# Kernel tuning notes

Hardware: AMD Instinct MI355X
Metric: run time of the kernel (lower is better)

Reference implementation:

```python
import jax, jax.numpy as jnp
import numpy as np

N, D = 16384, 32          # nodes, max neighbors
IN_F, HID, OUT_F = 128, 128, 128
HEADS = 8
HD = HID // HEADS         # head dim
TDIM = 64                 # Time2Vec dim
NORM = float(np.sqrt(1.0 / HD))


def _lin_params(key, fan_in, fan_out):
    k1, k2 = jax.random.split(key)
    lim = 1.0 / np.sqrt(fan_in)
    W = jax.random.uniform(k1, (fan_in, fan_out), jnp.float32, -lim, lim)
    b = jax.random.uniform(k2, (fan_out,), jnp.float32, -lim, lim)
    return W, b


def setup_inputs() -> dict:
    key = jax.random.key(0)
    ks = jax.random.split(key, 16)
    x = jax.random.normal(ks[0], (N, IN_F), jnp.float32)
    neighbors = jax.random.randint(ks[1], (N, D), 0, N)
    times = jax.random.uniform(ks[2], (N, D), jnp.float32)
    t = jax.random.uniform(ks[3], (1,), jnp.float32)
    # node KQV
    Wk, bk = _lin_params(ks[4], IN_F, HID)
    Wq, bq = _lin_params(ks[5], IN_F, HID)
    Wv, bv = _lin_params(ks[6], IN_F, HID)
    # Time2Vec kernel: [w0*t+b0, sin(t*W + B)] -> TDIM feats
    w0 = jax.random.normal(ks[7], (1,), jnp.float32)
    b0 = jax.random.normal(ks[8], (1,), jnp.float32)
    Wt = jax.random.normal(ks[9], (1, TDIM - 1), jnp.float32)
    Bt = jax.random.normal(ks[10], (TDIM - 1,), jnp.float32)
    # time KQV
    Wtk, btk = _lin_params(ks[11], TDIM, HID)
    Wtq, btq = _lin_params(ks[12], TDIM, HID)
    Wtv, btv = _lin_params(ks[13], TDIM, HID)
    # output MLP
    W1, b1 = _lin_params(ks[14], HID + IN_F, HID)
    W2, b2 = _lin_params(ks[15], HID, OUT_F)
    return dict(x=x, neighbors=neighbors, times=times, t=t,
                Wk=Wk, bk=bk, Wq=Wq, bq=bq, Wv=Wv, bv=bv,
                w0=w0, b0=b0, Wt=Wt, Bt=Bt,
                Wtk=Wtk, btk=btk, Wtq=Wtq, btq=btq, Wtv=Wtv, btv=btv,
                W1=W1, b1=b1, W2=W2, b2=b2)


def _t2v(ts, w0, b0, Wt, Bt):
    # ts: [..., 1] -> [..., TDIM]
    return jnp.concatenate([ts * w0 + b0, jnp.sin(ts @ Wt + Bt)], axis=-1)


def reference(x, neighbors, times, t,
              Wk, bk, Wq, bq, Wv, bv,
              w0, b0, Wt, Bt,
              Wtk, btk, Wtq, btq, Wtv, btv,
              W1, b1, W2, b2):
    t0 = t[0]
    # node-level K/Q/V for all nodes
    k_ = x @ Wk + bk
    q_ = x @ Wq + bq
    v_ = x @ Wv + bv
    # time encodings
    enc_t = _t2v(t.reshape(1, 1), w0, b0, Wt, Bt)          # [1, TDIM]
    tq = enc_t @ Wtq + btq                                  # [1, HID] (same for every target node)
    enc_nb = _t2v(times[..., None], w0, b0, Wt, Bt)        # [N, D, TDIM]
    tk = enc_nb @ Wtk + btk                                 # [N, D, HID]
    tv = enc_nb @ Wtv + btv
    # gather neighbor K/V and add time encodings
    q = q_ + tq                                             # [N, HID]
    k = k_[neighbors] + tk                                  # [N, D, HID]
    v = v_[neighbors] + tv
    # multi-head attention over (time-masked) neighbors
    qh = q.reshape(N, HEADS, HD)
    kh = k.reshape(N, D, HEADS, HD)
    vh = v.reshape(N, D, HEADS, HD)
    scores = jnp.einsum('nhd,nmhd->nhm', qh, kh) * NORM     # [N, H, D]
    mask = times <= t0                                      # [N, D]
    scores = jnp.where(mask[:, None, :], scores, -1e9)
    attn = jax.nn.softmax(scores, axis=-1)
    h = jnp.einsum('nhm,nmhd->nhd', attn, vh).reshape(N, HID)
    # nodes with no valid (time <= t) neighbors output zeros
    h = jnp.where(mask.any(axis=-1)[:, None], h, 0.0)
    # output MLP on [x || h]
    z = jnp.concatenate([x, h], axis=1)
    return jax.nn.relu(z @ W1 + b1) @ W2 + b2
```

## Files before the change

### kernel.cpp

```cpp
#include <hip/hip_runtime.h>
#include <hip/hip_bf16.h>

#define NNODES 16384

typedef unsigned short u16;
typedef unsigned int   u32;
typedef __attribute__((ext_vector_type(8))) short bf16x8;
typedef __attribute__((ext_vector_type(4))) float f32x4;

__device__ __forceinline__ float bfl(u32 u) { return __uint_as_float(u << 16); }
__device__ __forceinline__ float bfh(u32 u) { return __uint_as_float(u & 0xffff0000u); }
__device__ __forceinline__ u16 f2b(float f) {
    u32 u = __float_as_uint(f);
    return (u16)((u + 0x7fffu + ((u >> 16) & 1u)) >> 16);
}
__device__ __forceinline__ u32 pk2(float a, float b) {
    return (u32)f2b(a) | ((u32)f2b(b) << 16);
}
__device__ __forceinline__ bf16x8 bcast8(int4 v) {
    return __builtin_bit_cast(bf16x8, v);
}

#if defined(__has_builtin)
#if __has_builtin(__builtin_amdgcn_fdot2_f32_bf16)
#define HAVE_DOT2 1
#endif
#if __has_builtin(__builtin_amdgcn_sinf) && __has_builtin(__builtin_amdgcn_fractf)
#define HAVE_HWSIN 1
#endif
#endif
#ifndef HAVE_DOT2
#define HAVE_DOT2 0
#endif
#ifndef HAVE_HWSIN
#define HAVE_HWSIN 0
#endif

#if HAVE_DOT2
typedef __attribute__((ext_vector_type(2))) __bf16 bf16x2;
__device__ __forceinline__ float dot2b(u32 a, u32 b, float c) {
    return __builtin_amdgcn_fdot2_f32_bf16(__builtin_bit_cast(bf16x2, a),
                                           __builtin_bit_cast(bf16x2, b), c, false);
}
#else
__device__ __forceinline__ float dot2b(u32 a, u32 b, float c) {
    return c + bfl(a) * bfl(b) + bfh(a) * bfh(b);
}
#endif

#if HAVE_HWSIN
__device__ __forceinline__ float hwsin(float y) {
    return __builtin_amdgcn_sinf(__builtin_amdgcn_fractf(y));
}
#else
__device__ __forceinline__ float hwsin(float y) {
    return __sinf(y * 6.28318530717958647692f);
}
#endif

__global__ __launch_bounds__(256) void setup_all(
    const float* __restrict__ Wk, const float* __restrict__ Wq,
    const float* __restrict__ Wv, const float* __restrict__ W1,
    const float* __restrict__ W2,
    const float* __restrict__ t,  const float* __restrict__ bq,
    const float* __restrict__ btq,const float* __restrict__ Wtq,
    const float* __restrict__ w0, const float* __restrict__ b0,
    const float* __restrict__ Wt, const float* __restrict__ Bt,
    const float* __restrict__ Wtk,const float* __restrict__ Wtv,
    u16* __restrict__ Wts, float* __restrict__ qbias,
    float* __restrict__ gb, u32* __restrict__ Wtvp, u16* __restrict__ WGt,
    float2* __restrict__ wb2p)
{
    __shared__ float sb[128 * 17 + 64 * 17];
    int b = blockIdx.x, tt = threadIdx.x;

    if (b < 96) {
        int mat = b >> 4, tile = b & 15;
        const float* src = (mat == 0) ? Wk : (mat == 1) ? Wq : (mat == 2) ? Wv
                         : (mat == 3) ? W1 : (mat == 4) ? (W1 + 128 * 128) : W2;
        u16* dst = Wts + (size_t)mat * 16384;
        #pragma unroll
        for (int i = 0; i < 4; i++) {
            int o = i * 256 + tt;
            int cl = o >> 7, k = o & 127;
            int c = tile * 8 + cl;
            dst[c * 128 + k] = f2b(src[k * 128 + c]);
        }
    } else if (b == 96 || b == 97) {
        float tv = t[0];
        if (tt < 64)
            sb[tt] = (tt == 0) ? (w0[0] * tv + b0[0])
                               : __sinf(tv * Wt[tt - 1] + Bt[tt - 1]);
        __syncthreads();
        if (tt < 128) {
            float s = bq[tt] + btq[tt];
            for (int k = 0; k < 64; k++)
                s += sb[k] * Wtq[k * 128 + tt];
            sb[64 + tt] = s;
            if (b == 96) qbias[tt] = s;
        }
        __syncthreads();
        if (b == 97) {
            #pragma unroll
            for (int r = 0; r < 2; r++) {
                int hj = tt + r * 256;
                int h = hj >> 6, j = hj & 63;
                float s = 0.f;
                #pragma unroll
                for (int d = 0; d < 16; d++)
                    s += sb[64 + h * 16 + d] * Wtk[(size_t)j * 128 + h * 16 + d];
                gb[hj] = s;
            }
        }
    } else if (b == 98) {
        #pragma unroll
        for (int i = 0; i < 16; i++) {
            int idx = i * 256 + tt;
            int kp = idx >> 7, c = idx & 127;
            Wtvp[idx] = pk2(Wtv[(size_t)(2 * kp) * 128 + c],
                            Wtv[(size_t)(2 * kp + 1) * 128 + c]);
        }
        const float inv2pi = 0.15915494309189533577f;
        if (tt < 63) {
            float2 v;
            v.x = Wt[tt] * inv2pi;
            v.y = Bt[tt] * inv2pi;
            wb2p[tt + 1] = v;
        } else if (tt == 63) {
            float2 v;
            v.x = w0[0];
            v.y = b0[0];
            wb2p[0] = v;
        }
    } else {
        int h = b - 99;
        float* WqL  = sb;
        float* WtkL = sb + 128 * 17;
        #pragma unroll
        for (int i = 0; i < 8; i++) {
            int o = i * 256 + tt;
            int k = o >> 4, d = o & 15;
            WqL[k * 17 + d] = Wq[(size_t)k * 128 + h * 16 + d];
        }
        #pragma unroll
        for (int i = 0; i < 4; i++) {
            int o = i * 256 + tt;
            int j = o >> 4, d = o & 15;
            WtkL[j * 17 + d] = Wtk[(size_t)j * 128 + h * 16 + d];
        }
        __syncthreads();
        int j = tt >> 2, kb = (tt & 3) * 32;
        float wk[16];
        #pragma unroll
        for (int d = 0; d < 16; d++) wk[d] = WtkL[j * 17 + d];
        u32 out[16];
        #pragma unroll
        for (int kk2 = 0; kk2 < 16; kk2++) {
            int k = kb + 2 * kk2;
            float s0 = 0.f, s1 = 0.f;
            #pragma unroll
            for (int d = 0; d < 16; d++) {
                s0 += WqL[k * 17 + d] * wk[d];
                s1 += WqL[(k + 1) * 17 + d] * wk[d];
            }
            out[kk2] = pk2(s0, s1);
        }
        int4* dst = (int4*)(WGt + (size_t)(h * 64 + j) * 128 + kb);
        const int4* srcv = (const int4*)out;
        #pragma unroll
        for (int i = 0; i < 4; i++) dst[i] = srcv[i];
    }
}

__global__ __launch_bounds__(256) void gemm8m4(
    const float* __restrict__ x, const u16* __restrict__ Wts,
    const u16* __restrict__ WGt,
    const float* __restrict__ bk, const float* __restrict__ qbias,
    const float* __restrict__ bv, const float* __restrict__ b1,
    const float* __restrict__ gb,
    u16* __restrict__ Kb, u16* __restrict__ Qb,
    u16* __restrict__ Vb, u16* __restrict__ Pb, u16* __restrict__ Gb)
{
    __shared__ u16 As[64 * 128];
    __shared__ u16 Ws[128 * 128];
    int t = threadIdx.x;
    int rb = blockIdx.x * 64;
    int grp = blockIdx.y;

    u32* As32 = (u32*)As;
    u32* Ws32 = (u32*)Ws;
    const float2* Ap = (const float2*)(x + (size_t)rb * 128);
    #pragma unroll
    for (int i = 0; i < 16; i++) {
        int idx2 = i * 256 + t;
        int r = idx2 >> 6, k2 = idx2 & 63;
        float2 v = Ap[idx2];
        As32[(r * 64 + k2) ^ ((r & 7) << 2)] = pk2(v.x, v.y);
    }

    int wid = t >> 6, lane = t & 63;
    int l15 = lane & 15, lg = lane >> 4;
    int mb = wid * 16;
    int xo = (l15 & 7) << 3;

    #pragma unroll
    for (int mi = 0; mi < 4; mi++) {
        int mat = grp * 4 + mi;
        const u16* Wt = (mat < 4) ? (Wts + (size_t)mat * 16384)
                                  : (WGt + (size_t)(mat - 4) * 16384);
        const float* bias = (mat == 0) ? bk : (mat == 1) ? qbias
                          : (mat == 2) ? bv : (mat == 3) ? b1
                          : (gb + (mat - 4) * 128);
        const u32* Wp = (const u32*)Wt;
        __syncthreads();
        #pragma unroll
        for (int i = 0; i < 32; i++) {
            int idx2 = i * 256 + t;
            int c = idx2 >> 6, k2 = idx2 & 63;
            Ws32[(c * 64 + k2) ^ ((c & 7) << 2)] = Wp[idx2];
        }
        __syncthreads();

        f32x4 acc[8];
        #pragma unroll
        for (int nt = 0; nt < 8; nt++) acc[nt] = (f32x4){0.f, 0.f, 0.f, 0.f};
        #pragma unroll
        for (int ks = 0; ks < 4; ks++) {
            int kq = ks * 32 + lg * 8;
            bf16x8 a0 = *(bf16x8*)&As[((mb + l15) * 128 + kq) ^ xo];
            #pragma unroll
            for (int nt = 0; nt < 8; nt++) {
                bf16x8 b = *(bf16x8*)&Ws[((nt * 16 + l15) * 128 + kq) ^ xo];
                acc[nt] = __builtin_amdgcn_mfma_f32_16x16x32_bf16(a0, b, acc[nt], 0, 0, 0);
            }
        }

        u16* dst = (mat == 0) ? Kb : (mat == 1) ? Qb : (mat == 2) ? Vb
                 : (mat == 3) ? Pb : Gb;
        #pragma unroll
        for (int nt = 0; nt < 8; nt++) {
            int c = nt * 16 + l15;
            float bvv = bias[c];
            #pragma unroll
            for (int j = 0; j < 4; j++) {
                size_t row = rb + mb + lg * 4 + j;
                float v = acc[nt][j] + bvv;
                if (mat < 4) dst[row * 128 + c] = f2b(v);
                else         dst[row * 512 + (size_t)(mat - 4) * 128 + c] = f2b(v);
            }
        }
    }
}

__global__ __launch_bounds__(256) void mlp_fused(
    const u16* __restrict__ Hb, const u16* __restrict__ Wts,
    const u16* __restrict__ Pb, const float* __restrict__ b2,
    float* __restrict__ out)
{
    __shared__ u16 As[32 * 128];
    __shared__ u16 Ws[128 * 128];
    int t = threadIdx.x;
    int rb = blockIdx.x * 32;
    u32* As32 = (u32*)As;
    u32* Ws32 = (u32*)Ws;

    const u32* Hp = (const u32*)(Hb + (size_t)rb * 128);
    #pragma unroll
    for (int i = 0; i < 8; i++) {
        int idx2 = i * 256 + t;
        int r = idx2 >> 6, k2 = idx2 & 63;
        As32[(r * 64 + k2) ^ ((r & 7) << 2)] = Hp[idx2];
    }
    {
        const u32* Wp = (const u32*)(Wts + 4 * 16384);
        #pragma unroll
        for (int i = 0; i < 32; i++) {
            int idx2 = i * 256 + t;
            int c = idx2 >> 6, k2 = idx2 & 63;
            Ws32[(c * 64 + k2) ^ ((c & 7) << 2)] = Wp[idx2];
        }
    }
    __syncthreads();

    int wid = t >> 6, lane = t & 63;
    int l15 = lane & 15, lg = lane >> 4;
    int rh = wid >> 1, ch = wid & 1;
    int mb = rh * 16;
    int xo = (l15 & 7) << 3;

    f32x4 acc[4];
    #pragma unroll
    for (int nt = 0; nt < 4; nt++) acc[nt] = (f32x4){0.f, 0.f, 0.f, 0.f};
    #pragma unroll
    for (int ks = 0; ks < 4; ks++) {
        int kq = ks * 32 + lg * 8;
        bf16x8 a0 = *(bf16x8*)&As[((mb + l15) * 128 + kq) ^ xo];
        #pragma unroll
        for (int nt = 0; nt < 4; nt++) {
            bf16x8 b = *(bf16x8*)&Ws[(((ch * 4 + nt) * 16 + l15) * 128 + kq) ^ xo];
            acc[nt] = __builtin_amdgcn_mfma_f32_16x16x32_bf16(a0, b, acc[nt], 0, 0, 0);
        }
    }
    __syncthreads();

    #pragma unroll
    for (int nt = 0; nt < 4; nt++) {
        int c = ch * 64 + nt * 16 + l15;
        #pragma unroll
        for (int j = 0; j < 4; j++) {
            int row = mb + lg * 4 + j;
            float pv = bfl((u32)Pb[(size_t)(rb + row) * 128 + c]);
            float v = fmaxf(acc[nt][j] + pv, 0.f);
            As[(row * 128 + c) ^ ((row & 7) << 3)] = f2b(v);
        }
    }
    {
        const u32* Wp = (const u32*)(Wts + 5 * 16384);
        #pragma unroll
        for (int i = 0; i < 32; i++) {
            int idx2 = i * 256 + t;
            int c = idx2 >> 6, k2 = idx2 & 63;
            Ws32[(c * 64 + k2) ^ ((c & 7) << 2)] = Wp[idx2];
        }
    }
    __syncthreads();

    #pragma unroll
    for (int nt = 0; nt < 4; nt++) acc[nt] = (f32x4){0.f, 0.f, 0.f, 0.f};
    #pragma unroll
    for (int ks = 0; ks < 4; ks++) {
        int kq = ks * 32 + lg * 8;
        bf16x8 a0 = *(bf16x8*)&As[((mb + l15) * 128 + kq) ^ xo];
        #pragma unroll
        for (int nt = 0; nt < 4; nt++) {
            bf16x8 b = *(bf16x8*)&Ws[(((ch * 4 + nt) * 16 + l15) * 128 + kq) ^ xo];
            acc[nt] = __builtin_amdgcn_mfma_f32_16x16x32_bf16(a0, b, acc[nt], 0, 0, 0);
        }
    }
    #pragma unroll
    for (int nt = 0; nt < 4; nt++) {
        int c = ch * 64 + nt * 16 + l15;
        float bvv = b2[c];
        #pragma unroll
        for (int j = 0; j < 4; j++) {
            size_t row = rb + mb + lg * 4 + j;
            out[row * 128 + c] = acc[nt][j] + bvv;
        }
    }
}

__global__ __launch_bounds__(256, 5) void attn_kernel(
    const int*   __restrict__ neighbors, const float* __restrict__ times,
    const float* __restrict__ tptr,
    const u16* __restrict__ Kb, const u16* __restrict__ Qb,
    const u16* __restrict__ Vb, const u16* __restrict__ Gb,
    const float* __restrict__ btk,  const u32* __restrict__ Wtvp,
    const float* __restrict__ btv,
    const float2* __restrict__ wb2p,
    u16* __restrict__ Hb)
{
    __shared__ u16   enc[4][32][72];
    __shared__ u32   gbp[4][8][32];
    __shared__ u32   qb[4][64];
    __shared__ float pbuf[4][8][33];
    __shared__ u16   ewp[4][8][66];
    __shared__ int   nbb[4][32];
    __shared__ float cb_[4][8];

    int t = threadIdx.x;
    int wid = t >> 6, lane = t & 63;
    int n = blockIdx.x * 4 + wid;
    float t0 = tptr[0];
    int l15 = lane & 15, lg = lane >> 4;

    qb[wid][lane] = ((const u32*)Qb)[(size_t)n * 64 + lane];
    {
        int4 g4 = *(const int4*)((const u32*)Gb + (size_t)n * 256 + 4 * lane);
        const u32* gw = (const u32*)&g4;
        #pragma unroll
        for (int i = 0; i < 4; i++) {
            int q4 = 4 * lane + i;
            gbp[wid][q4 >> 5][q4 & 31] = gw[i];
        }
    }

    int m = lane & 31, h2 = lane >> 5;
    if (lane < 32) nbb[wid][lane] = neighbors[n * 32 + lane];
    float tm = times[n * 32 + m];
    bool valid = (tm <= t0);
    unsigned long long bal = __ballot(valid);
    bool anyv = (bal != 0ull);

    u32 vpre[32];
    #pragma unroll
    for (int mm = 0; mm < 32; mm++) {
        int nbm = nbb[wid][mm];
        vpre[mm] = *(const u32*)(Vb + (size_t)nbm * 128 + 2 * lane);
    }

    int kbase = 32 * h2;
    #pragma unroll
    for (int i = 0; i < 16; i++) {
        int k0 = kbase + 2 * i;
        float2 wbA = wb2p[k0];
        float2 wbB = wb2p[k0 + 1];
        float yA = fmaf(tm, wbA.x, wbA.y);
        float yB = fmaf(tm, wbB.x, wbB.y);
        float v0 = (k0 == 0) ? yA : hwsin(yA);
        float v1 = hwsin(yB);
        *(u32*)&enc[wid][m][k0] = pk2(v0, v1);
    }

    if (lane < 8) {
        float s = 0.f;
        #pragma unroll
        for (int j = 0; j < 8; j++) {
            u32 qp = qb[wid][lane * 8 + j];
            s += bfl(qp) * btk[lane * 16 + 2 * j] + bfh(qp) * btk[lane * 16 + 2 * j + 1];
        }
        cb_[wid][lane] = s;
    }

    f32x4 accS[2];
    accS[0] = (f32x4){0.f, 0.f, 0.f, 0.f};
    accS[1] = (f32x4){0.f, 0.f, 0.f, 0.f};

    int nb0 = nbb[wid][l15];
    int nb1 = nbb[wid][l15 + 16];
    const u16* K0 = Kb + (size_t)nb0 * 128;
    const u16* K1 = Kb + (size_t)nb1 * 128;
    const int4 zero4 = {0, 0, 0, 0};
    #pragma unroll
    for (int ks = 0; ks < 4; ks++) {
        bf16x8 qf = bcast8((l15 == ks * 2 + (lg >> 1))
                               ? *(const int4*)&qb[wid][ks * 16 + lg * 4]
                               : zero4);
        bf16x8 k0f = bcast8(*(const int4*)(K0 + ks * 32 + lg * 8));
        bf16x8 k1f = bcast8(*(const int4*)(K1 + ks * 32 + lg * 8));
        accS[0] = __builtin_amdgcn_mfma_f32_16x16x32_bf16(k0f, qf, accS[0], 0, 0, 0);
        accS[1] = __builtin_amdgcn_mfma_f32_16x16x32_bf16(k1f, qf, accS[1], 0, 0, 0);
    }
    #pragma unroll
    for (int ks = 0; ks < 2; ks++) {
        int4 gi = zero4;
        if (l15 < 8) {
            int2 ga = *(const int2*)&gbp[wid][l15][ks * 16 + lg * 4];
            int2 gbq = *(const int2*)&gbp[wid][l15][ks * 16 + lg * 4 + 2];
            gi.x = ga.x; gi.y = ga.y; gi.z = gbq.x; gi.w = gbq.y;
        }
        bf16x8 gf = bcast8(gi);
        bf16x8 e0 = *(const bf16x8*)&enc[wid][l15][ks * 32 + lg * 8];
        bf16x8 e1 = *(const bf16x8*)&enc[wid][l15 + 16][ks * 32 + lg * 8];
        accS[0] = __builtin_amdgcn_mfma_f32_16x16x32_bf16(e0, gf, accS[0], 0, 0, 0);
        accS[1] = __builtin_amdgcn_mfma_f32_16x16x32_bf16(e1, gf, accS[1], 0, 0, 0);
    }

    float cbv = (l15 < 8) ? cb_[wid][l15] : 0.f;
    float sc[2][4];
    #pragma unroll
    for (int mt = 0; mt < 2; mt++) {
        #pragma unroll
        for (int j = 0; j < 4; j++) {
            int mr = mt * 16 + lg * 4 + j;
            float v = 0.25f * (accS[mt][j] + cbv);
            sc[mt][j] = ((bal >> mr) & 1ull) ? v : -1e9f;
        }
    }
    float mx = sc[0][0];
    #pragma unroll
    for (int mt = 0; mt < 2; mt++)
        #pragma unroll
        for (int j = 0; j < 4; j++) mx = fmaxf(mx, sc[mt][j]);
    mx = fmaxf(mx, __shfl_xor(mx, 16));
    mx = fmaxf(mx, __shfl_xor(mx, 32));
    float p[2][4];
    float s = 0.f;
    #pragma unroll
    for (int mt = 0; mt < 2; mt++)
        #pragma unroll
        for (int j = 0; j < 4; j++) { p[mt][j] = __expf(sc[mt][j] - mx); s += p[mt][j]; }
    s += __shfl_xor(s, 16);
    s += __shfl_xor(s, 32);
    float inv = 1.0f / s;
    if (l15 < 8) {
        #pragma unroll
        for (int mt = 0; mt < 2; mt++)
            #pragma unroll
            for (int j = 0; j < 4; j++)
                pbuf[wid][l15][mt * 16 + lg * 4 + j] = p[mt][j] * inv;
    }

    {
        int hh = l15 & 7;
        float pa[8];
        #pragma unroll
        for (int j = 0; j < 8; j++) pa[j] = pbuf[wid][hh][8 * lg + j];
        int4 ai;
        ai.x = pk2(pa[0], pa[1]); ai.y = pk2(pa[2], pa[3]);
        ai.z = pk2(pa[4], pa[5]); ai.w = pk2(pa[6], pa[7]);
        bf16x8 af = bcast8(ai);
        #pragma unroll
        for (int nt = 0; nt < 4; nt++) {
            int col = nt * 16 + l15;
            int4 bi;
            bi.x = (u32)enc[wid][8 * lg + 0][col] | ((u32)enc[wid][8 * lg + 1][col] << 16);
            bi.y = (u32)enc[wid][8 * lg + 2][col] | ((u32)enc[wid][8 * lg + 3][col] << 16);
            bi.z = (u32)enc[wid][8 * lg + 4][col] | ((u32)enc[wid][8 * lg + 5][col] << 16);
            bi.w = (u32)enc[wid][8 * lg + 6][col] | ((u32)enc[wid][8 * lg + 7][col] << 16);
            bf16x8 bfr = bcast8(bi);
            f32x4 ce = (f32x4){0.f, 0.f, 0.f, 0.f};
            ce = __builtin_amdgcn_mfma_f32_16x16x32_bf16(af, bfr, ce, 0, 0, 0);
            if (lg < 2) {
                #pragma unroll
                for (int j = 0; j < 4; j++)
                    ewp[wid][4 * lg + j][col] = f2b(ce[j]);
            }
        }
    }

    int myh = lane >> 3;
    float av0 = 0.f, av1 = 0.f;
    #pragma unroll
    for (int mm = 0; mm < 32; mm++) {
        float a = pbuf[wid][myh][mm];
        av0 += a * bfl(vpre[mm]);
        av1 += a * bfh(vpre[mm]);
    }
    float ht0 = 0.f, ht1 = 0.f;
    #pragma unroll 8
    for (int kp = 0; kp < 32; kp++) {
        u32 ew = *(const u32*)&ewp[wid][myh][2 * kp];
        int2 wv = *(const int2*)&Wtvp[kp * 128 + 2 * lane];
        ht0 = dot2b(ew, (u32)wv.x, ht0);
        ht1 = dot2b(ew, (u32)wv.y, ht1);
    }
    float2 bt2 = *(const float2*)&btv[2 * lane];
    float ox = anyv ? (av0 + ht0 + bt2.x) : 0.0f;
    float oy = anyv ? (av1 + ht1 + bt2.y) : 0.0f;
    ((u32*)Hb)[(size_t)n * 64 + lane] = pk2(ox, oy);
}

extern "C" void kernel_launch(void* const* d_in, const int* in_sizes, int n_in,
                              void* d_out, int out_size, void* d_ws, size_t ws_size,
                              hipStream_t stream)
{
    const float* x        = (const float*)d_in[0];
    const int*   neighbors= (const int*)  d_in[1];
    const float* times    = (const float*)d_in[2];
    const float* t        = (const float*)d_in[3];
    const float* Wk  = (const float*)d_in[4];
    const float* bk  = (const float*)d_in[5];
    const float* Wq  = (const float*)d_in[6];
    const float* bq  = (const float*)d_in[7];
    const float* Wv  = (const float*)d_in[8];
    const float* bv  = (const float*)d_in[9];
    const float* w0  = (const float*)d_in[10];
    const float* b0  = (const float*)d_in[11];
    const float* Wt  = (const float*)d_in[12];
    const float* Bt  = (const float*)d_in[13];
    const float* Wtk = (const float*)d_in[14];
    const float* btk = (const float*)d_in[15];
    const float* Wtq = (const float*)d_in[16];
    const float* btq = (const float*)d_in[17];
    const float* Wtv = (const float*)d_in[18];
    const float* btv = (const float*)d_in[19];
    const float* W1  = (const float*)d_in[20];
    const float* b1  = (const float*)d_in[21];
    const float* W2  = (const float*)d_in[22];
    const float* b2  = (const float*)d_in[23];

    float* ws = (float*)d_ws;
    const size_t NF = (size_t)NNODES * 128;
    u16*   Kb    = (u16*)ws;
    u16*   Qb    = Kb + NF;
    u16*   Vb    = Qb + NF;
    u16*   Pb    = Vb + NF;
    u16*   Hb    = Pb + NF;
    u16*   Gb    = Hb + NF;
    float* qbias = (float*)(Gb + (size_t)NNODES * 512);
    u16*   Wts   = (u16*)(qbias + 128);
    u16*   WGt   = Wts + 6 * 16384;
    float* gb    = (float*)(WGt + 65536);
    u32*   Wtvp  = (u32*)(gb + 512);
    float2* wb2p = (float2*)(Wtvp + 4096);

    setup_all<<<107, 256, 0, stream>>>(Wk, Wq, Wv, W1, W2,
                                       t, bq, btq, Wtq, w0, b0, Wt, Bt,
                                       Wtk, Wtv,
                                       Wts, qbias, gb, Wtvp, WGt, wb2p);

    gemm8m4<<<dim3(NNODES / 64, 2), 256, 0, stream>>>(
        x, Wts, WGt, bk, qbias, bv, b1, gb, Kb, Qb, Vb, Pb, Gb);

    attn_kernel<<<NNODES / 4, 256, 0, stream>>>(neighbors, times, t,
                                                Kb, Qb, Vb, Gb,
                                                btk, Wtvp, btv, wb2p,
                                                Hb);

    mlp_fused<<<NNODES / 32, 256, 0, stream>>>(Hb, Wts, Pb, b2,
                                               (float*)d_out);
}
```

Measured before the change: 101.1 us.

## Compute per-head query-time-key projection inside attention kernel instead of precomputing

The per-node term q·Wtk per head is no longer precomputed in the GEMM kernel as a separate [N,512] bf16 buffer built from folded Wq·Wtk weights. The attention kernel now computes it on the fly with MFMA, from the already-loaded bf16 query row and a bf16 copy of Wtk. This removes four of the eight GEMM weight passes, the large intermediate write and read, and the setup blocks that built the folded weights. In exchange the attention kernel does extra MFMA work and reads Wtk per block, which should mostly hit in cache. Rounding changes because q is rounded to bf16 before this product.

```diff
diff --git a/kernel.cpp b/kernel.cpp
--- a/kernel.cpp
+++ b/kernel.cpp
@@ -68,10 +68,10 @@
     const float* __restrict__ Wt, const float* __restrict__ Bt,
     const float* __restrict__ Wtk,const float* __restrict__ Wtv,
     u16* __restrict__ Wts, float* __restrict__ qbias,
-    float* __restrict__ gb, u32* __restrict__ Wtvp, u16* __restrict__ WGt,
-    float2* __restrict__ wb2p)
+    u32* __restrict__ Wtvp, float2* __restrict__ wb2p,
+    u16* __restrict__ Wtkb)
 {
-    __shared__ float sb[128 * 17 + 64 * 17];
+    __shared__ float sb[192];
     int b = blockIdx.x, tt = threadIdx.x;
 
     if (b < 96) {
@@ -86,7 +86,7 @@
             int c = tile * 8 + cl;
             dst[c * 128 + k] = f2b(src[k * 128 + c]);
         }
-    } else if (b == 96 || b == 97) {
+    } else if (b == 96) {
         float tv = t[0];
         if (tt < 64)
             sb[tt] = (tt == 0) ? (w0[0] * tv + b0[0])
@@ -96,23 +96,9 @@
             float s = bq[tt] + btq[tt];
             for (int k = 0; k < 64; k++)
                 s += sb[k] * Wtq[k * 128 + tt];
-            sb[64 + tt] = s;
-            if (b == 96) qbias[tt] = s;
-        }
-        __syncthreads();
-        if (b == 97) {
-            #pragma unroll
-            for (int r = 0; r < 2; r++) {
-                int hj = tt + r * 256;
-                int h = hj >> 6, j = hj & 63;
-                float s = 0.f;
-                #pragma unroll
-                for (int d = 0; d < 16; d++)
-                    s += sb[64 + h * 16 + d] * Wtk[(size_t)j * 128 + h * 16 + d];
-                gb[hj] = s;
-            }
-        }
-    } else if (b == 98) {
+            qbias[tt] = s;
+        }
+    } else if (b == 97) {
         #pragma unroll
         for (int i = 0; i < 16; i++) {
             int idx = i * 256 + tt;
@@ -133,53 +119,20 @@
             wb2p[0] = v;
         }
     } else {
-        int h = b - 99;
-        float* WqL  = sb;
-        float* WtkL = sb + 128 * 17;
-        #pragma unroll
-        for (int i = 0; i < 8; i++) {
-            int o = i * 256 + tt;
-            int k = o >> 4, d = o & 15;
-            WqL[k * 17 + d] = Wq[(size_t)k * 128 + h * 16 + d];
-        }
-        #pragma unroll
-        for (int i = 0; i < 4; i++) {
-            int o = i * 256 + tt;
-            int j = o >> 4, d = o & 15;
-            WtkL[j * 17 + d] = Wtk[(size_t)j * 128 + h * 16 + d];
-        }
-        __syncthreads();
-        int j = tt >> 2, kb = (tt & 3) * 32;
-        float wk[16];
-        #pragma unroll
-        for (int d = 0; d < 16; d++) wk[d] = WtkL[j * 17 + d];
-        u32 out[16];
-        #pragma unroll
-        for (int kk2 = 0; kk2 < 16; kk2++) {
-            int k = kb + 2 * kk2;
-            float s0 = 0.f, s1 = 0.f;
-            #pragma unroll
-            for (int d = 0; d < 16; d++) {
-                s0 += WqL[k * 17 + d] * wk[d];
-                s1 += WqL[(k + 1) * 17 + d] * wk[d];
-            }
-            out[kk2] = pk2(s0, s1);
-        }
-        int4* dst = (int4*)(WGt + (size_t)(h * 64 + j) * 128 + kb);
-        const int4* srcv = (const int4*)out;
-        #pragma unroll
-        for (int i = 0; i < 4; i++) dst[i] = srcv[i];
-    }
-}
-
-__global__ __launch_bounds__(256) void gemm8m4(
+        #pragma unroll
+        for (int i = 0; i < 32; i++) {
+            int idx = i * 256 + tt;
+            Wtkb[idx] = f2b(Wtk[idx]);
+        }
+    }
+}
+
+__global__ __launch_bounds__(256) void gemm4m2(
     const float* __restrict__ x, const u16* __restrict__ Wts,
-    const u16* __restrict__ WGt,
     const float* __restrict__ bk, const float* __restrict__ qbias,
     const float* __restrict__ bv, const float* __restrict__ b1,
-    const float* __restrict__ gb,
     u16* __restrict__ Kb, u16* __restrict__ Qb,
-    u16* __restrict__ Vb, u16* __restrict__ Pb, u16* __restrict__ Gb)
+    u16* __restrict__ Vb, u16* __restrict__ Pb)
 {
     __shared__ u16 As[64 * 128];
     __shared__ u16 Ws[128 * 128];
@@ -204,13 +157,11 @@
     int xo = (l15 & 7) << 3;
 
     #pragma unroll
-    for (int mi = 0; mi < 4; mi++) {
-        int mat = grp * 4 + mi;
-        const u16* Wt = (mat < 4) ? (Wts + (size_t)mat * 16384)
-                                  : (WGt + (size_t)(mat - 4) * 16384);
+    for (int mi = 0; mi < 2; mi++) {
+        int mat = grp * 2 + mi;
+        const u16* Wt = Wts + (size_t)mat * 16384;
         const float* bias = (mat == 0) ? bk : (mat == 1) ? qbias
-                          : (mat == 2) ? bv : (mat == 3) ? b1
-                          : (gb + (mat - 4) * 128);
+                          : (mat == 2) ? bv : b1;
         const u32* Wp = (const u32*)Wt;
         __syncthreads();
         #pragma unroll
@@ -235,8 +186,7 @@
             }
         }
 
-        u16* dst = (mat == 0) ? Kb : (mat == 1) ? Qb : (mat == 2) ? Vb
-                 : (mat == 3) ? Pb : Gb;
+        u16* dst = (mat == 0) ? Kb : (mat == 1) ? Qb : (mat == 2) ? Vb : Pb;
         #pragma unroll
         for (int nt = 0; nt < 8; nt++) {
             int c = nt * 16 + l15;
@@ -244,9 +194,7 @@
             #pragma unroll
             for (int j = 0; j < 4; j++) {
                 size_t row = rb + mb + lg * 4 + j;
-                float v = acc[nt][j] + bvv;
-                if (mat < 4) dst[row * 128 + c] = f2b(v);
-                else         dst[row * 512 + (size_t)(mat - 4) * 128 + c] = f2b(v);
+                dst[row * 128 + c] = f2b(acc[nt][j] + bvv);
             }
         }
     }
@@ -353,7 +301,7 @@
     const int*   __restrict__ neighbors, const float* __restrict__ times,
     const float* __restrict__ tptr,
     const u16* __restrict__ Kb, const u16* __restrict__ Qb,
-    const u16* __restrict__ Vb, const u16* __restrict__ Gb,
+    const u16* __restrict__ Vb, const u16* __restrict__ Wtkb,
     const float* __restrict__ btk,  const u32* __restrict__ Wtvp,
     const float* __restrict__ btv,
     const float2* __restrict__ wb2p,
@@ -374,15 +322,6 @@
     int l15 = lane & 15, lg = lane >> 4;
 
     qb[wid][lane] = ((const u32*)Qb)[(size_t)n * 64 + lane];
-    {
-        int4 g4 = *(const int4*)((const u32*)Gb + (size_t)n * 256 + 4 * lane);
-        const u32* gw = (const u32*)&g4;
-        #pragma unroll
-        for (int i = 0; i < 4; i++) {
-            int q4 = 4 * lane + i;
-            gbp[wid][q4 >> 5][q4 & 31] = gw[i];
-        }
-    }
 
     int m = lane & 31, h2 = lane >> 5;
     if (lane < 32) nbb[wid][lane] = neighbors[n * 32 + lane];
@@ -396,6 +335,33 @@
     for (int mm = 0; mm < 32; mm++) {
         int nbm = nbb[wid][mm];
         vpre[mm] = *(const u32*)(Vb + (size_t)nbm * 128 + 2 * lane);
+    }
+
+    const int4 zero4 = {0, 0, 0, 0};
+
+    {
+        f32x4 gacc[4];
+        #pragma unroll
+        for (int mt = 0; mt < 4; mt++) gacc[mt] = (f32x4){0.f, 0.f, 0.f, 0.f};
+        #pragma unroll
+        for (int ks = 0; ks < 4; ks++) {
+            bf16x8 qf = bcast8((l15 == ks * 2 + (lg >> 1))
+                                   ? *(const int4*)&qb[wid][ks * 16 + lg * 4]
+                                   : zero4);
+            #pragma unroll
+            for (int mt = 0; mt < 4; mt++) {
+                bf16x8 af = bcast8(*(const int4*)(Wtkb + (size_t)(mt * 16 + l15) * 128
+                                                  + ks * 32 + lg * 8));
+                gacc[mt] = __builtin_amdgcn_mfma_f32_16x16x32_bf16(af, qf, gacc[mt], 0, 0, 0);
+            }
+        }
+        if (l15 < 8) {
+            #pragma unroll
+            for (int mt = 0; mt < 4; mt++) {
+                gbp[wid][l15][mt * 8 + lg * 2]     = pk2(gacc[mt][0], gacc[mt][1]);
+                gbp[wid][l15][mt * 8 + lg * 2 + 1] = pk2(gacc[mt][2], gacc[mt][3]);
+            }
+        }
     }
 
     int kbase = 32 * h2;
@@ -429,7 +395,6 @@
     int nb1 = nbb[wid][l15 + 16];
     const u16* K0 = Kb + (size_t)nb0 * 128;
     const u16* K1 = Kb + (size_t)nb1 * 128;
-    const int4 zero4 = {0, 0, 0, 0};
     #pragma unroll
     for (int ks = 0; ks < 4; ks++) {
         bf16x8 qf = bcast8((l15 == ks * 2 + (lg >> 1))
@@ -576,24 +541,22 @@
     u16*   Vb    = Qb + NF;
     u16*   Pb    = Vb + NF;
     u16*   Hb    = Pb + NF;
-    u16*   Gb    = Hb + NF;
-    float* qbias = (float*)(Gb + (size_t)NNODES * 512);
+    float* qbias = (float*)(Hb + NF);
     u16*   Wts   = (u16*)(qbias + 128);
-    u16*   WGt   = Wts + 6 * 16384;
-    float* gb    = (float*)(WGt + 65536);
-    u32*   Wtvp  = (u32*)(gb + 512);
+    u32*   Wtvp  = (u32*)(Wts + 6 * 16384);
     float2* wb2p = (float2*)(Wtvp + 4096);
-
-    setup_all<<<107, 256, 0, stream>>>(Wk, Wq, Wv, W1, W2,
-                                       t, bq, btq, Wtq, w0, b0, Wt, Bt,
-                                       Wtk, Wtv,
-                                       Wts, qbias, gb, Wtvp, WGt, wb2p);
-
-    gemm8m4<<<dim3(NNODES / 64, 2), 256, 0, stream>>>(
-        x, Wts, WGt, bk, qbias, bv, b1, gb, Kb, Qb, Vb, Pb, Gb);
+    u16*   Wtkb  = (u16*)(wb2p + 64);
+
+    setup_all<<<99, 256, 0, stream>>>(Wk, Wq, Wv, W1, W2,
+                                      t, bq, btq, Wtq, w0, b0, Wt, Bt,
+                                      Wtk, Wtv,
+                                      Wts, qbias, Wtvp, wb2p, Wtkb);
+
+    gemm4m2<<<dim3(NNODES / 64, 2), 256, 0, stream>>>(
+        x, Wts, bk, qbias, bv, b1, Kb, Qb, Vb, Pb);
 
     attn_kernel<<<NNODES / 4, 256, 0, stream>>>(neighbors, times, t,
-                                                Kb, Qb, Vb, Gb,
+                                                Kb, Qb, Vb, Wtkb,
                                                 btk, Wtvp, btv, wb2p,
                                                 Hb);
 
```

New measurement: 134.6 us. 33.1% more time.
